# Optimization experiments

Measured on AMD Instinct MI355X. Metric: run time of the kernel, lower is better.

Reference implementation:

```python
import jax, jax.numpy as jnp
import numpy as np

N_NODES = 100000
N_EDGES = 6400000
D_FEAT = 8
# Fuzzy inference system: 3 Gaussian membership functions per input
# (negative / zero / positive linguistic terms), 3x3 = 9 rules per edge.
MF_CENTERS = jnp.array([-1.0, 0.0, 1.0], dtype=jnp.float32)
MF_SIGMA = 0.5


def setup_inputs() -> dict:
    key = jax.random.key(0)
    k1, k2, k3, k4 = jax.random.split(key, 4)
    feat = jax.random.normal(k1, (N_NODES, D_FEAT), dtype=jnp.float32)
    edge_src = jax.random.randint(k2, (N_EDGES,), 0, N_NODES, dtype=jnp.int32)
    edge_dst = jax.random.randint(k3, (N_EDGES,), 0, N_NODES, dtype=jnp.int32)
    etypes = jax.random.randint(k4, (N_EDGES,), 0, 4, dtype=jnp.int32)
    return {"feat": feat, "edge_src": edge_src, "edge_dst": edge_dst, "etypes": etypes}


def _ante_generator(h_src, h_dst):
    # Relative-coordinate antecedent inputs (first two feature dims are coords).
    x1 = h_dst[:, 0] - h_src[:, 0]  # [E]
    x2 = h_dst[:, 1] - h_src[:, 1]  # [E]
    return x1, x2


def _fuzzy_infer_sys(x1, x2):
    inv2s2 = 1.0 / (2.0 * MF_SIGMA * MF_SIGMA)
    mu1 = jnp.exp(-((x1[:, None] - MF_CENTERS) ** 2) * inv2s2)  # [E, 3]
    mu2 = jnp.exp(-((x2[:, None] - MF_CENTERS) ** 2) * inv2s2)  # [E, 3]
    # Rule firing strengths: outer product of memberships -> [E, 9]
    ante = (mu1[:, :, None] * mu2[:, None, :]).reshape(-1, 9)
    return ante


def reference(feat, edge_src, edge_dst, etypes):
    # apply_edges: gather src/dst node features per edge
    h_src = feat[edge_src]  # [E, D]
    h_dst = feat[edge_dst]  # [E, D]
    x1, x2 = _ante_generator(h_src, h_dst)
    ante = _fuzzy_infer_sys(x1, x2)  # [E, 9] stored in g.edata['ante']
    return ante
```

## Files before the change

### kernel.cpp

```cpp
#include <hip/hip_runtime.h>


#define TPB 256

typedef float  f2 __attribute__((ext_vector_type(2)));
typedef float  f4 __attribute__((ext_vector_type(4)));
typedef int    i2 __attribute__((ext_vector_type(2)));

__global__ __launch_bounds__(TPB, 8) void ante_kernel(
    const float* __restrict__ feat,
    const int*   __restrict__ esrc,
    const int*   __restrict__ edst,
    float*       __restrict__ out,
    int e2,
    int nf4)
{
    __shared__ float lds[TPB * 18];
    const int tid = threadIdx.x;
    const int t   = blockIdx.x * TPB + tid;

    if (t < e2) {
        const i2 s2 = __builtin_nontemporal_load(reinterpret_cast<const i2*>(esrc) + t);
        const i2 d2 = __builtin_nontemporal_load(reinterpret_cast<const i2*>(edst) + t);

        const f2 fs0 = *reinterpret_cast<const f2*>(feat + (size_t)s2.x * 8);
        const f2 fd0 = *reinterpret_cast<const f2*>(feat + (size_t)d2.x * 8);
        const f2 fs1 = *reinterpret_cast<const f2*>(feat + (size_t)s2.y * 8);
        const f2 fd1 = *reinterpret_cast<const f2*>(feat + (size_t)d2.y * 8);

        float res[18];
#pragma unroll
        for (int q = 0; q < 2; ++q) {
            const float x1 = (q == 0) ? (fd0.x - fs0.x) : (fd1.x - fs1.x);
            const float x2 = (q == 0) ? (fd0.y - fs0.y) : (fd1.y - fs1.y);

            float m1[3], m2[3];
            {
                const float a = x1 + 1.0f, c = x1 - 1.0f;
                m1[0] = __expf(-2.0f * a * a);
                m1[1] = __expf(-2.0f * x1 * x1);
                m1[2] = __expf(-2.0f * c * c);
            }
            {
                const float a = x2 + 1.0f, c = x2 - 1.0f;
                m2[0] = __expf(-2.0f * a * a);
                m2[1] = __expf(-2.0f * x2 * x2);
                m2[2] = __expf(-2.0f * c * c);
            }
#pragma unroll
            for (int i = 0; i < 3; ++i)
#pragma unroll
                for (int j = 0; j < 3; ++j)
                    res[q * 9 + i * 3 + j] = m1[i] * m2[j];
        }

        f2* my2 = reinterpret_cast<f2*>(lds) + tid * 9;
#pragma unroll
        for (int k = 0; k < 9; ++k) {
            f2 v; v.x = res[2 * k]; v.y = res[2 * k + 1];
            my2[k] = v;
        }
    }
    __syncthreads();

    const size_t blk_f4 = (size_t)blockIdx.x * (TPB * 9 / 2);
    f4* out4 = reinterpret_cast<f4*>(out);
    const f4* lds4 = reinterpret_cast<const f4*>(lds);

#pragma unroll
    for (int k = 0; k < 5; ++k) {
        const int f = k * TPB + tid;
        if (f < TPB * 9 / 2) {
            const size_t g = blk_f4 + (size_t)f;
            if (g < (size_t)nf4)
                __builtin_nontemporal_store(lds4[f], out4 + g);
        }
    }
}

extern "C" void kernel_launch(void* const* d_in, const int* in_sizes, int n_in,
                              void* d_out, int out_size, void* d_ws, size_t ws_size,
                              hipStream_t stream) {
    const float* feat = (const float*)d_in[0];
    const int*   esrc = (const int*)d_in[1];
    const int*   edst = (const int*)d_in[2];
    float* out = (float*)d_out;

    const int E   = in_sizes[1];
    const int e2  = E / 2;
    const int nf4 = out_size / 4;
    const int grid = (e2 + TPB - 1) / TPB;
    ante_kernel<<<grid, TPB, 0, stream>>>(feat, esrc, edst, out, e2, nf4);
}
```

Measured before the change: 97.28 us.

## Split gather and membership compute into two kernels via workspace

Splits the fused kernel into a gather kernel, which writes per-edge coordinate differences to a workspace buffer, and a compute kernel, which reads them back and produces the 9 rule strengths. The aim is to separate the latency-bound random gather from the store-heavy compute phase so each kernel runs at better occupancy. The cost is an extra 51 MB round trip through the workspace and a second launch. If the workspace is too small, the code falls back to the original fused kernel.

```diff
diff --git a/kernel.cpp b/kernel.cpp
--- a/kernel.cpp
+++ b/kernel.cpp
@@ -7,33 +7,39 @@
 typedef float  f4 __attribute__((ext_vector_type(4)));
 typedef int    i2 __attribute__((ext_vector_type(2)));
 
-__global__ __launch_bounds__(TPB, 8) void ante_kernel(
+__global__ __launch_bounds__(TPB) void gather_kernel(
     const float* __restrict__ feat,
     const int*   __restrict__ esrc,
     const int*   __restrict__ edst,
-    float*       __restrict__ out,
-    int e2,
-    int nf4)
+    f2*          __restrict__ ws2,
+    int E)
+{
+    const int e = blockIdx.x * TPB + threadIdx.x;
+    if (e >= E) return;
+    const int s = __builtin_nontemporal_load(esrc + e);
+    const int d = __builtin_nontemporal_load(edst + e);
+    const f2 fs = *reinterpret_cast<const f2*>(feat + (size_t)s * 8);
+    const f2 fd = *reinterpret_cast<const f2*>(feat + (size_t)d * 8);
+    f2 x; x.x = fd.x - fs.x; x.y = fd.y - fs.y;
+    __builtin_nontemporal_store(x, ws2 + e);
+}
+
+__global__ __launch_bounds__(TPB, 8) void compute_kernel(
+    const f4* __restrict__ ws4,
+    float*    __restrict__ out,
+    int e2, int nf4)
 {
     __shared__ float lds[TPB * 18];
     const int tid = threadIdx.x;
     const int t   = blockIdx.x * TPB + tid;
 
     if (t < e2) {
-        const i2 s2 = __builtin_nontemporal_load(reinterpret_cast<const i2*>(esrc) + t);
-        const i2 d2 = __builtin_nontemporal_load(reinterpret_cast<const i2*>(edst) + t);
-
-        const f2 fs0 = *reinterpret_cast<const f2*>(feat + (size_t)s2.x * 8);
-        const f2 fd0 = *reinterpret_cast<const f2*>(feat + (size_t)d2.x * 8);
-        const f2 fs1 = *reinterpret_cast<const f2*>(feat + (size_t)s2.y * 8);
-        const f2 fd1 = *reinterpret_cast<const f2*>(feat + (size_t)d2.y * 8);
-
+        const f4 x = __builtin_nontemporal_load(ws4 + t);
         float res[18];
 #pragma unroll
         for (int q = 0; q < 2; ++q) {
-            const float x1 = (q == 0) ? (fd0.x - fs0.x) : (fd1.x - fs1.x);
-            const float x2 = (q == 0) ? (fd0.y - fs0.y) : (fd1.y - fs1.y);
-
+            const float x1 = (q == 0) ? x.x : x.z;
+            const float x2 = (q == 0) ? x.y : x.w;
             float m1[3], m2[3];
             {
                 const float a = x1 + 1.0f, c = x1 - 1.0f;
@@ -53,7 +59,6 @@
                 for (int j = 0; j < 3; ++j)
                     res[q * 9 + i * 3 + j] = m1[i] * m2[j];
         }
-
         f2* my2 = reinterpret_cast<f2*>(lds) + tid * 9;
 #pragma unroll
         for (int k = 0; k < 9; ++k) {
@@ -66,7 +71,71 @@
     const size_t blk_f4 = (size_t)blockIdx.x * (TPB * 9 / 2);
     f4* out4 = reinterpret_cast<f4*>(out);
     const f4* lds4 = reinterpret_cast<const f4*>(lds);
+#pragma unroll
+    for (int k = 0; k < 5; ++k) {
+        const int f = k * TPB + tid;
+        if (f < TPB * 9 / 2) {
+            const size_t g = blk_f4 + (size_t)f;
+            if (g < (size_t)nf4)
+                __builtin_nontemporal_store(lds4[f], out4 + g);
+        }
+    }
+}
 
+__global__ __launch_bounds__(TPB, 8) void ante_fused(
+    const float* __restrict__ feat,
+    const int*   __restrict__ esrc,
+    const int*   __restrict__ edst,
+    float*       __restrict__ out,
+    int e2, int nf4)
+{
+    __shared__ float lds[TPB * 18];
+    const int tid = threadIdx.x;
+    const int t   = blockIdx.x * TPB + tid;
+
+    if (t < e2) {
+        const i2 s2 = __builtin_nontemporal_load(reinterpret_cast<const i2*>(esrc) + t);
+        const i2 d2 = __builtin_nontemporal_load(reinterpret_cast<const i2*>(edst) + t);
+        const f2 fs0 = *reinterpret_cast<const f2*>(feat + (size_t)s2.x * 8);
+        const f2 fd0 = *reinterpret_cast<const f2*>(feat + (size_t)d2.x * 8);
+        const f2 fs1 = *reinterpret_cast<const f2*>(feat + (size_t)s2.y * 8);
+        const f2 fd1 = *reinterpret_cast<const f2*>(feat + (size_t)d2.y * 8);
+        float res[18];
+#pragma unroll
+        for (int q = 0; q < 2; ++q) {
+            const float x1 = (q == 0) ? (fd0.x - fs0.x) : (fd1.x - fs1.x);
+            const float x2 = (q == 0) ? (fd0.y - fs0.y) : (fd1.y - fs1.y);
+            float m1[3], m2[3];
+            {
+                const float a = x1 + 1.0f, c = x1 - 1.0f;
+                m1[0] = __expf(-2.0f * a * a);
+                m1[1] = __expf(-2.0f * x1 * x1);
+                m1[2] = __expf(-2.0f * c * c);
+            }
+            {
+                const float a = x2 + 1.0f, c = x2 - 1.0f;
+                m2[0] = __expf(-2.0f * a * a);
+                m2[1] = __expf(-2.0f * x2 * x2);
+                m2[2] = __expf(-2.0f * c * c);
+            }
+#pragma unroll
+            for (int i = 0; i < 3; ++i)
+#pragma unroll
+                for (int j = 0; j < 3; ++j)
+                    res[q * 9 + i * 3 + j] = m1[i] * m2[j];
+        }
+        f2* my2 = reinterpret_cast<f2*>(lds) + tid * 9;
+#pragma unroll
+        for (int k = 0; k < 9; ++k) {
+            f2 v; v.x = res[2 * k]; v.y = res[2 * k + 1];
+            my2[k] = v;
+        }
+    }
+    __syncthreads();
+
+    const size_t blk_f4 = (size_t)blockIdx.x * (TPB * 9 / 2);
+    f4* out4 = reinterpret_cast<f4*>(out);
+    const f4* lds4 = reinterpret_cast<const f4*>(lds);
 #pragma unroll
     for (int k = 0; k < 5; ++k) {
         const int f = k * TPB + tid;
@@ -89,6 +158,13 @@
     const int E   = in_sizes[1];
     const int e2  = E / 2;
     const int nf4 = out_size / 4;
-    const int grid = (e2 + TPB - 1) / TPB;
-    ante_kernel<<<grid, TPB, 0, stream>>>(feat, esrc, edst, out, e2, nf4);
+
+    if (ws_size >= (size_t)E * 2 * sizeof(float)) {
+        f2* ws2 = (f2*)d_ws;
+        gather_kernel<<<(E + TPB - 1) / TPB, TPB, 0, stream>>>(feat, esrc, edst, ws2, E);
+        compute_kernel<<<(e2 + TPB - 1) / TPB, TPB, 0, stream>>>(
+            reinterpret_cast<const f4*>(ws2), out, e2, nf4);
+    } else {
+        ante_fused<<<(e2 + TPB - 1) / TPB, TPB, 0, stream>>>(feat, esrc, edst, out, e2, nf4);
+    }
 }
```

Measured after the change: 116.6 us. +19.9%, slower.

## Process four edge tiles per block with batched index and gather loads

Applied to the files above, without the earlier changes.

Each block now handles four tiles of 512 edges. All index loads and all feature gathers are issued up front so more memory requests are in flight per thread, and the LDS staging buffer is reused per tile for the coalesced output stores. Launch bounds drop to 4 blocks per SM and the bounds checks are removed, so correctness relies on E being divisible by 2048. That holds for 6.4M edges but would drop the tail for other sizes.

```diff
diff --git a/kernel.cpp b/kernel.cpp
--- a/kernel.cpp
+++ b/kernel.cpp
@@ -2,38 +2,52 @@
 
 
 #define TPB 256
+#define TILES 4
 
 typedef float  f2 __attribute__((ext_vector_type(2)));
 typedef float  f4 __attribute__((ext_vector_type(4)));
 typedef int    i2 __attribute__((ext_vector_type(2)));
 
-__global__ __launch_bounds__(TPB, 8) void ante_kernel(
+__global__ __launch_bounds__(TPB, 4) void ante_kernel(
     const float* __restrict__ feat,
     const int*   __restrict__ esrc,
     const int*   __restrict__ edst,
-    float*       __restrict__ out,
-    int e2,
-    int nf4)
+    float*       __restrict__ out)
 {
     __shared__ float lds[TPB * 18];
     const int tid = threadIdx.x;
-    const int t   = blockIdx.x * TPB + tid;
+    const size_t blk_e0 = (size_t)blockIdx.x * (TPB * TILES * 2);
 
-    if (t < e2) {
-        const i2 s2 = __builtin_nontemporal_load(reinterpret_cast<const i2*>(esrc) + t);
-        const i2 d2 = __builtin_nontemporal_load(reinterpret_cast<const i2*>(edst) + t);
+    i2 s[TILES], d[TILES];
+#pragma unroll
+    for (int p = 0; p < TILES; ++p) {
+        const size_t base = blk_e0 + (size_t)p * (TPB * 2) + 2 * tid;
+        s[p] = __builtin_nontemporal_load(reinterpret_cast<const i2*>(esrc + base));
+        d[p] = __builtin_nontemporal_load(reinterpret_cast<const i2*>(edst + base));
+    }
 
-        const f2 fs0 = *reinterpret_cast<const f2*>(feat + (size_t)s2.x * 8);
-        const f2 fd0 = *reinterpret_cast<const f2*>(feat + (size_t)d2.x * 8);
-        const f2 fs1 = *reinterpret_cast<const f2*>(feat + (size_t)s2.y * 8);
-        const f2 fd1 = *reinterpret_cast<const f2*>(feat + (size_t)d2.y * 8);
+    f2 g[TILES][4];
+#pragma unroll
+    for (int p = 0; p < TILES; ++p) {
+        g[p][0] = *reinterpret_cast<const f2*>(feat + (size_t)s[p].x * 8);
+        g[p][1] = *reinterpret_cast<const f2*>(feat + (size_t)d[p].x * 8);
+        g[p][2] = *reinterpret_cast<const f2*>(feat + (size_t)s[p].y * 8);
+        g[p][3] = *reinterpret_cast<const f2*>(feat + (size_t)d[p].y * 8);
+    }
 
+    f4* out4 = reinterpret_cast<f4*>(out);
+    const f4* lds4 = reinterpret_cast<const f4*>(lds);
+    const size_t blk_f4 = (size_t)blockIdx.x * (TPB * TILES * 2 * 9 / 4);
+
+#pragma unroll
+    for (int p = 0; p < TILES; ++p) {
         float res[18];
 #pragma unroll
         for (int q = 0; q < 2; ++q) {
-            const float x1 = (q == 0) ? (fd0.x - fs0.x) : (fd1.x - fs1.x);
-            const float x2 = (q == 0) ? (fd0.y - fs0.y) : (fd1.y - fs1.y);
-
+            const f2 fsv = g[p][2 * q];
+            const f2 fdv = g[p][2 * q + 1];
+            const float x1 = fdv.x - fsv.x;
+            const float x2 = fdv.y - fsv.y;
             float m1[3], m2[3];
             {
                 const float a = x1 + 1.0f, c = x1 - 1.0f;
@@ -54,26 +68,21 @@
                     res[q * 9 + i * 3 + j] = m1[i] * m2[j];
         }
 
+        if (p > 0) __syncthreads();
         f2* my2 = reinterpret_cast<f2*>(lds) + tid * 9;
 #pragma unroll
         for (int k = 0; k < 9; ++k) {
             f2 v; v.x = res[2 * k]; v.y = res[2 * k + 1];
             my2[k] = v;
         }
-    }
-    __syncthreads();
+        __syncthreads();
 
-    const size_t blk_f4 = (size_t)blockIdx.x * (TPB * 9 / 2);
-    f4* out4 = reinterpret_cast<f4*>(out);
-    const f4* lds4 = reinterpret_cast<const f4*>(lds);
-
+        const size_t tile_f4 = blk_f4 + (size_t)p * (TPB * 2 * 9 / 4);
 #pragma unroll
-    for (int k = 0; k < 5; ++k) {
-        const int f = k * TPB + tid;
-        if (f < TPB * 9 / 2) {
-            const size_t g = blk_f4 + (size_t)f;
-            if (g < (size_t)nf4)
-                __builtin_nontemporal_store(lds4[f], out4 + g);
+        for (int k = 0; k < 5; ++k) {
+            const int f = k * TPB + tid;
+            if (f < TPB * 9 / 2)
+                __builtin_nontemporal_store(lds4[f], out4 + tile_f4 + f);
         }
     }
 }
@@ -86,9 +95,8 @@
     const int*   edst = (const int*)d_in[2];
     float* out = (float*)d_out;
 
-    const int E   = in_sizes[1];
-    const int e2  = E / 2;
-    const int nf4 = out_size / 4;
-    const int grid = (e2 + TPB - 1) / TPB;
-    ante_kernel<<<grid, TPB, 0, stream>>>(feat, esrc, edst, out, e2, nf4);
+    const int E = in_sizes[1];
+    const int edges_per_block = TPB * TILES * 2;
+    const int grid = E / edges_per_block;
+    ante_kernel<<<grid, TPB, 0, stream>>>(feat, esrc, edst, out);
 }
```

New measurement: 109.4 us. 12.5% more time.

## Use persistent grid-stride blocks with software-pipelined index and gather prefetch

Applied to the files above, without the earlier changes.

Replaces the one-tile-per-block launch with a persistent grid capped at 2048 blocks. Each block loops over tiles and prefetches the next tile's edge indices and feature gathers while it computes and stores the current one. The aim is to hide gather latency and cut block launch overhead. Tail handling is dropped: ntiles = E/512, so any E not divisible by 512 would leave trailing edges unprocessed. The extra syncthreads per tile also adds overhead.

```diff
diff --git a/kernel.cpp b/kernel.cpp
--- a/kernel.cpp
+++ b/kernel.cpp
@@ -7,74 +7,99 @@
 typedef float  f4 __attribute__((ext_vector_type(4)));
 typedef int    i2 __attribute__((ext_vector_type(2)));
 
+__device__ __forceinline__ void load_idx(const int* __restrict__ esrc,
+                                         const int* __restrict__ edst,
+                                         int t, int tid, i2& s, i2& d) {
+    const size_t base = (size_t)t * (TPB * 2) + 2 * tid;
+    s = __builtin_nontemporal_load(reinterpret_cast<const i2*>(esrc + base));
+    d = __builtin_nontemporal_load(reinterpret_cast<const i2*>(edst + base));
+}
+
+__device__ __forceinline__ void gath(const float* __restrict__ feat,
+                                     const i2 s, const i2 d, f2 g[4]) {
+    g[0] = *reinterpret_cast<const f2*>(feat + (size_t)s.x * 8);
+    g[1] = *reinterpret_cast<const f2*>(feat + (size_t)d.x * 8);
+    g[2] = *reinterpret_cast<const f2*>(feat + (size_t)s.y * 8);
+    g[3] = *reinterpret_cast<const f2*>(feat + (size_t)d.y * 8);
+}
+
+__device__ __forceinline__ void memb(float x, float m[3]) {
+    const float a = x + 1.0f, c = x - 1.0f;
+    m[0] = __expf(-2.0f * a * a);
+    m[1] = __expf(-2.0f * x * x);
+    m[2] = __expf(-2.0f * c * c);
+}
+
+__device__ __forceinline__ void compute_store(const f2 g[4], int t, int tid,
+                                              float* lds, float* __restrict__ out) {
+    float m1a[3], m2a[3], m1b[3], m2b[3];
+    memb(g[1].x - g[0].x, m1a);
+    memb(g[1].y - g[0].y, m2a);
+    memb(g[3].x - g[2].x, m1b);
+    memb(g[3].y - g[2].y, m2b);
+
+    __syncthreads();
+    f2* my2 = reinterpret_cast<f2*>(lds) + tid * 9;
+    f2 v;
+    v.x = m1a[0] * m2a[0]; v.y = m1a[0] * m2a[1]; my2[0] = v;
+    v.x = m1a[0] * m2a[2]; v.y = m1a[1] * m2a[0]; my2[1] = v;
+    v.x = m1a[1] * m2a[1]; v.y = m1a[1] * m2a[2]; my2[2] = v;
+    v.x = m1a[2] * m2a[0]; v.y = m1a[2] * m2a[1]; my2[3] = v;
+    v.x = m1a[2] * m2a[2]; v.y = m1b[0] * m2b[0]; my2[4] = v;
+    v.x = m1b[0] * m2b[1]; v.y = m1b[0] * m2b[2]; my2[5] = v;
+    v.x = m1b[1] * m2b[0]; v.y = m1b[1] * m2b[1]; my2[6] = v;
+    v.x = m1b[1] * m2b[2]; v.y = m1b[2] * m2b[0]; my2[7] = v;
+    v.x = m1b[2] * m2b[1]; v.y = m1b[2] * m2b[2]; my2[8] = v;
+    __syncthreads();
+
+    const f4* lds4 = reinterpret_cast<const f4*>(lds);
+    f4* out4 = reinterpret_cast<f4*>(out);
+    const size_t tf4 = (size_t)t * (TPB * 9 / 2);
+#pragma unroll
+    for (int k = 0; k < 5; ++k) {
+        const int f = k * TPB + tid;
+        if (f < TPB * 9 / 2)
+            __builtin_nontemporal_store(lds4[f], out4 + tf4 + f);
+    }
+}
+
 __global__ __launch_bounds__(TPB, 8) void ante_kernel(
     const float* __restrict__ feat,
     const int*   __restrict__ esrc,
     const int*   __restrict__ edst,
     float*       __restrict__ out,
-    int e2,
-    int nf4)
+    int ntiles)
 {
     __shared__ float lds[TPB * 18];
     const int tid = threadIdx.x;
-    const int t   = blockIdx.x * TPB + tid;
+    const int G   = gridDim.x;
 
-    if (t < e2) {
-        const i2 s2 = __builtin_nontemporal_load(reinterpret_cast<const i2*>(esrc) + t);
-        const i2 d2 = __builtin_nontemporal_load(reinterpret_cast<const i2*>(edst) + t);
+    int t = blockIdx.x;
+    if (t >= ntiles) return;
 
-        const f2 fs0 = *reinterpret_cast<const f2*>(feat + (size_t)s2.x * 8);
-        const f2 fd0 = *reinterpret_cast<const f2*>(feat + (size_t)d2.x * 8);
-        const f2 fs1 = *reinterpret_cast<const f2*>(feat + (size_t)s2.y * 8);
-        const f2 fd1 = *reinterpret_cast<const f2*>(feat + (size_t)d2.y * 8);
+    i2 sA, dA, sB, dB;
+    f2 gA[4], gB[4];
 
-        float res[18];
-#pragma unroll
-        for (int q = 0; q < 2; ++q) {
-            const float x1 = (q == 0) ? (fd0.x - fs0.x) : (fd1.x - fs1.x);
-            const float x2 = (q == 0) ? (fd0.y - fs0.y) : (fd1.y - fs1.y);
+    load_idx(esrc, edst, t, tid, sA, dA);
+    gath(feat, sA, dA, gA);
+    int t2 = t + G;
+    bool vB = t2 < ntiles;
+    if (vB) load_idx(esrc, edst, t2, tid, sB, dB);
 
-            float m1[3], m2[3];
-            {
-                const float a = x1 + 1.0f, c = x1 - 1.0f;
-                m1[0] = __expf(-2.0f * a * a);
-                m1[1] = __expf(-2.0f * x1 * x1);
-                m1[2] = __expf(-2.0f * c * c);
-            }
-            {
-                const float a = x2 + 1.0f, c = x2 - 1.0f;
-                m2[0] = __expf(-2.0f * a * a);
-                m2[1] = __expf(-2.0f * x2 * x2);
-                m2[2] = __expf(-2.0f * c * c);
-            }
-#pragma unroll
-            for (int i = 0; i < 3; ++i)
-#pragma unroll
-                for (int j = 0; j < 3; ++j)
-                    res[q * 9 + i * 3 + j] = m1[i] * m2[j];
-        }
+    for (;;) {
+        if (vB) gath(feat, sB, dB, gB);
+        int t3 = t2 + G; bool v3 = t3 < ntiles;
+        if (v3) load_idx(esrc, edst, t3, tid, sA, dA);
+        compute_store(gA, t, tid, lds, out);
+        if (!vB) break;
+        t = t2; t2 = t3; vB = v3;
 
-        f2* my2 = reinterpret_cast<f2*>(lds) + tid * 9;
-#pragma unroll
-        for (int k = 0; k < 9; ++k) {
-            f2 v; v.x = res[2 * k]; v.y = res[2 * k + 1];
-            my2[k] = v;
-        }
-    }
-    __syncthreads();
-
-    const size_t blk_f4 = (size_t)blockIdx.x * (TPB * 9 / 2);
-    f4* out4 = reinterpret_cast<f4*>(out);
-    const f4* lds4 = reinterpret_cast<const f4*>(lds);
-
-#pragma unroll
-    for (int k = 0; k < 5; ++k) {
-        const int f = k * TPB + tid;
-        if (f < TPB * 9 / 2) {
-            const size_t g = blk_f4 + (size_t)f;
-            if (g < (size_t)nf4)
-                __builtin_nontemporal_store(lds4[f], out4 + g);
-        }
+        if (vB) gath(feat, sA, dA, gA);
+        t3 = t2 + G; v3 = t3 < ntiles;
+        if (v3) load_idx(esrc, edst, t3, tid, sB, dB);
+        compute_store(gB, t, tid, lds, out);
+        if (!vB) break;
+        t = t2; t2 = t3; vB = v3;
     }
 }
 
@@ -86,9 +111,8 @@
     const int*   edst = (const int*)d_in[2];
     float* out = (float*)d_out;
 
-    const int E   = in_sizes[1];
-    const int e2  = E / 2;
-    const int nf4 = out_size / 4;
-    const int grid = (e2 + TPB - 1) / TPB;
-    ante_kernel<<<grid, TPB, 0, stream>>>(feat, esrc, edst, out, e2, nf4);
+    const int E = in_sizes[1];
+    const int ntiles = E / (TPB * 2);
+    const int grid = (ntiles < 2048) ? ntiles : 2048;
+    ante_kernel<<<grid, TPB, 0, stream>>>(feat, esrc, edst, out, ntiles);
 }
```

Result: slower. 110.6 us (+13.7%).
